# Kernel optimization log

Measured on AMD Instinct MI355X. Metric: run time of the kernel, lower is better.

The kernel has to match this reference:

```python
import jax, jax.numpy as jnp
import numpy as np

H = 64        # index_n_heads
D = 128       # index_head_dim
R = 64        # rope_head_dim
TOPK = 512    # index_topk
FP8_MAX = 448.0
EPS = 1e-6
THETA = 10000.0


def setup_inputs() -> dict:
    key = jax.random.key(0)
    ks = jax.random.split(key, 6)
    T, DM, QL = 1536, 7168, 1536
    return {
        "hidden_states": jax.random.normal(ks[0], (T, DM), jnp.float32),
        "q_lora": jax.random.normal(ks[1], (T, QL), jnp.float32),
        "wq_b": jax.random.normal(ks[2], (QL, H * D), jnp.float32) / np.sqrt(QL),
        "wk": jax.random.normal(ks[3], (DM, D), jnp.float32) / np.sqrt(DM),
        "k_norm_w": jnp.ones((D,), jnp.float32),
        "k_norm_b": jnp.zeros((D,), jnp.float32),
        "weights_proj_w": jax.random.normal(ks[4], (DM, H), jnp.float32) / np.sqrt(DM),
        "positions": jnp.arange(T, dtype=jnp.int32),
    }


def _rope_neox(x, pos):
    # x: [T, ..., R]; pos: [T]. NEOX-style (half-split) rotary on the rope slice.
    half = R // 2
    inv = 1.0 / (THETA ** (jnp.arange(half, dtype=jnp.float32) / half))
    ang = pos.astype(jnp.float32)[:, None] * inv  # [T, half]
    cos, sin = jnp.cos(ang), jnp.sin(ang)
    while cos.ndim < x.ndim:
        cos, sin = cos[:, None, :], sin[:, None, :]
    x1, x2 = x[..., :half], x[..., half:]
    return jnp.concatenate([x1 * cos - x2 * sin, x2 * cos + x1 * sin], axis=-1)


def _fp8_quant(x):
    # per-row (last-dim) e4m3 quantization: value -> fp8 payload + fp32 scale
    scale = jnp.maximum(jnp.max(jnp.abs(x), axis=-1, keepdims=True) / FP8_MAX, 1e-12)
    xq = (x / scale).astype(jnp.float8_e4m3fn).astype(jnp.float32)
    return xq, scale


def reference(hidden_states, q_lora, wq_b, wk, k_norm_w, k_norm_b, weights_proj_w, positions):
    T = hidden_states.shape[0]
    softmax_scale = D ** (-0.5)
    weights_scale = H ** (-0.5)

    # projections
    q = (q_lora @ wq_b).reshape(T, H, D)          # wq_b
    k = hidden_states @ wk                        # wk

    # k_norm (LayerNorm)
    mu = jnp.mean(k, axis=-1, keepdims=True)
    var = jnp.mean((k - mu) ** 2, axis=-1, keepdims=True)
    k = (k - mu) * jax.lax.rsqrt(var + EPS) * k_norm_w + k_norm_b

    # RoPE on the first rope_head_dim dims of q and k
    q = jnp.concatenate([_rope_neox(q[..., :R], positions), q[..., R:]], axis=-1)
    k = jnp.concatenate([_rope_neox(k[..., :R], positions), k[..., R:]], axis=-1)

    # fp8 quantization (per token-head for q, per token for k)
    q_fp8, q_scale = _fp8_quant(q)   # [T,H,D], [T,H,1]
    k_fp8, k_scale = _fp8_quant(k)   # [T,D],   [T,1]

    # head-gate weights: weights_proj(x) * q_scale * softmax_scale * weights_scale
    gate = hidden_states @ weights_proj_w                      # [T,H]
    w = gate[..., None] * q_scale * (softmax_scale * weights_scale)  # [T,H,1]

    # index score: I[t,s] = sum_h w[t,h] * relu(q[t,h] . k[s]) * k_scale[s]
    qk = jnp.einsum('thd,sd->ths', q_fp8, k_fp8)               # [T,H,S]
    score = jnp.einsum('th,ths->ts', w[..., 0], jax.nn.relu(qk))
    score = score * k_scale[:, 0][None, :]

    # causal (ragged prefill) mask + topk block selection
    causal = positions[:, None] >= positions[None, :]
    score = jnp.where(causal, score, -jnp.inf)
    vals, idx = jax.lax.top_k(score, TOPK)
    idx = jnp.where(jnp.isfinite(vals), idx, -1)
    return idx, vals
```

## Files before the change

kernel.cpp:

```cpp
#include <hip/hip_runtime.h>
#include <hip/hip_bf16.h>
#include <math.h>

#define T_SZ 1536
#define DM_SZ 7168
#define QL_SZ 1536
#define H_SZ 64
#define D_SZ 128
#define ND 8192
#define TOPK_SZ 512
#define N2 192
#define SPLITK2 16

typedef float f32x4 __attribute__((ext_vector_type(4)));
typedef short s16x8 __attribute__((ext_vector_type(8)));
typedef unsigned long long u64;

static __device__ __forceinline__ unsigned char f32_to_e4m3(float x){
  unsigned int b = __float_as_uint(x);
  unsigned int s = (b >> 24) & 0x80u;
  float a = fabsf(x);
  if (a < 0.015625f){
    int m = (int)rintf(a * 512.0f);
    if (m == 8) return (unsigned char)(s | 0x08u);
    return (unsigned char)(s | (unsigned)m);
  }
  int e;
  float mant = frexpf(a, &e);
  int E = e - 1;
  int m = (int)rintf(mant * 16.0f) - 8;
  if (m == 8){ E += 1; m = 0; }
  if (E > 8 || (E == 8 && m > 6)) return (unsigned char)(s | 0x7Eu);
  return (unsigned char)(s | ((unsigned)(E + 7) << 3) | (unsigned)m);
}

static __device__ __forceinline__ unsigned short bf16_rne(float x){
  unsigned int u = __float_as_uint(x);
  return (unsigned short)((u + 0x7FFFu + ((u >> 16) & 1u)) >> 16);
}

typedef __attribute__((address_space(1))) const void gas_void;
typedef __attribute__((address_space(3))) void las_void;
static __device__ __forceinline__ void stage16(const void* g, void* l){
  __builtin_amdgcn_global_load_lds((gas_void*)g, (las_void*)l, 16, 0, 0);
}

__global__ void rope_table_k(const int* __restrict__ pos, float* __restrict__ cs){
  int i = blockIdx.x * blockDim.x + threadIdx.x;
  if (i >= T_SZ * 32) return;
  int t = i >> 5, j = i & 31;
  float inv = 1.0f / powf(10000.0f, (float)j * (1.0f / 32.0f));
  float ang = (float)pos[t] * inv;
  cs[t * 64 + j]      = cosf(ang);
  cs[t * 64 + 32 + j] = sinf(ang);
}

__global__ __launch_bounds__(256) void conv_split_k(const float* __restrict__ A,
                                                    unsigned short* __restrict__ hi,
                                                    unsigned short* __restrict__ lo,
                                                    int n4){
  int i = blockIdx.x * 256 + threadIdx.x;
  if (i >= n4) return;
  float4 v = *(const float4*)&A[(size_t)i * 4];
  float f[4] = {v.x, v.y, v.z, v.w};
  unsigned short hb[4], lb[4];
#pragma unroll
  for (int j = 0; j < 4; ++j){
    hb[j] = bf16_rne(f[j]);
    float hf = __uint_as_float((unsigned int)hb[j] << 16);
    lb[j] = bf16_rne(f[j] - hf);
  }
  ushort4 h, l;
  h.x = hb[0]; h.y = hb[1]; h.z = hb[2]; h.w = hb[3];
  l.x = lb[0]; l.y = lb[1]; l.z = lb[2]; l.w = lb[3];
  *(ushort4*)&hi[(size_t)i * 4] = h;
  *(ushort4*)&lo[(size_t)i * 4] = l;
}

__global__ __launch_bounds__(256) void convB_k(const float* __restrict__ B,
                                               unsigned short* __restrict__ bhi,
                                               unsigned short* __restrict__ blo){
  __shared__ float ld[32][33];
  const int n0 = blockIdx.x * 32, k0 = blockIdx.y * 32;
  const int t = threadIdx.x;
  const int r = t >> 3, c4 = (t & 7) * 4;
  float4 v = *(const float4*)&B[(size_t)(k0 + r) * ND + n0 + c4];
  ld[r][c4 + 0] = v.x; ld[r][c4 + 1] = v.y; ld[r][c4 + 2] = v.z; ld[r][c4 + 3] = v.w;
  __syncthreads();
  unsigned short hb[4], lb[4];
#pragma unroll
  for (int j = 0; j < 4; ++j){
    float x = ld[c4 + j][r];
    hb[j] = bf16_rne(x);
    float hf = __uint_as_float((unsigned int)hb[j] << 16);
    lb[j] = bf16_rne(x - hf);
  }
  ushort4 h, l;
  h.x = hb[0]; h.y = hb[1]; h.z = hb[2]; h.w = hb[3];
  l.x = lb[0]; l.y = lb[1]; l.z = lb[2]; l.w = lb[3];
  *(ushort4*)&bhi[(size_t)(n0 + r) * QL_SZ + k0 + c4] = h;
  *(ushort4*)&blo[(size_t)(n0 + r) * QL_SZ + k0 + c4] = l;
}

__global__ __launch_bounds__(256) void conv_w2_k(const float* __restrict__ wk,
                                                 const float* __restrict__ wp,
                                                 unsigned short* __restrict__ bhi,
                                                 unsigned short* __restrict__ blo){
  __shared__ float ld[32][33];
  const int n0 = blockIdx.x * 32, k0 = blockIdx.y * 32;
  const int t = threadIdx.x;
  const int r = t >> 3, c4 = (t & 7) * 4;
  float4 v;
  if (n0 < 128) v = *(const float4*)&wk[(size_t)(k0 + r) * 128 + n0 + c4];
  else          v = *(const float4*)&wp[(size_t)(k0 + r) * 64 + (n0 - 128) + c4];
  ld[r][c4 + 0] = v.x; ld[r][c4 + 1] = v.y; ld[r][c4 + 2] = v.z; ld[r][c4 + 3] = v.w;
  __syncthreads();
  unsigned short hb[4], lb[4];
#pragma unroll
  for (int j = 0; j < 4; ++j){
    float x = ld[c4 + j][r];
    hb[j] = bf16_rne(x);
    float hf = __uint_as_float((unsigned int)hb[j] << 16);
    lb[j] = bf16_rne(x - hf);
  }
  ushort4 h, l;
  h.x = hb[0]; h.y = hb[1]; h.z = hb[2]; h.w = hb[3];
  l.x = lb[0]; l.y = lb[1]; l.z = lb[2]; l.w = lb[3];
  *(ushort4*)&bhi[(size_t)(n0 + r) * DM_SZ + k0 + c4] = h;
  *(ushort4*)&blo[(size_t)(n0 + r) * DM_SZ + k0 + c4] = l;
}

__global__ __launch_bounds__(256) void gemm1_mfma_k(const unsigned short* __restrict__ Ahi,
                                                    const unsigned short* __restrict__ Alo,
                                                    const unsigned short* __restrict__ Bhi,
                                                    const unsigned short* __restrict__ Blo,
                                                    float* __restrict__ C){
  __shared__ unsigned short As [128 * 64];
  __shared__ unsigned short Bs0[128 * 64];
  __shared__ unsigned short Bs1[128 * 64];
  const int bid = blockIdx.x;
  const int lid = (bid & 7) * 96 + (bid >> 3);
  const int mt = lid % 12, nt = lid / 12;
  const int m0 = mt * 128, n0 = nt * 128;
  const int tid = threadIdx.x;
  const int w = tid >> 6, l = tid & 63;
  const int wr = w >> 1, wc = w & 1;
  const int lr = l & 15, lg = l >> 4;

  const int srow = w * 32 + (l >> 3);
  const int ssl  = (l & 7) ^ ((l >> 3) & 7);
  const size_t gA = (size_t)(m0 + srow) * QL_SZ + ssl * 8;
  const size_t gB = (size_t)(n0 + srow) * QL_SZ + ssl * 8;
  const int lbase = w * 2048;

  f32x4 acc[4][4];
#pragma unroll
  for (int i = 0; i < 4; ++i)
#pragma unroll
    for (int j = 0; j < 4; ++j) acc[i][j] = (f32x4){0.f, 0.f, 0.f, 0.f};

  const int amrow = wr * 64 + lr;
  const int bnrow = wc * 64 + lr;

  for (int k0 = 0; k0 < QL_SZ; k0 += 64){
#pragma unroll
    for (int i = 0; i < 4; ++i){
      size_t go = (size_t)i * 8 * QL_SZ + k0;
      stage16(Ahi + gA + go, As  + lbase + i * 512);
      stage16(Bhi + gB + go, Bs0 + lbase + i * 512);
      stage16(Blo + gB + go, Bs1 + lbase + i * 512);
    }
    __syncthreads();
#pragma unroll
    for (int kk = 0; kk < 2; ++kk){
      s16x8 af[4], b0[4], b1[4];
#pragma unroll
      for (int f = 0; f < 4; ++f){
        int ma = amrow + f * 16;
        int nb = bnrow + f * 16;
        int sa = ((kk * 4 + lg) ^ (ma & 7)) * 16;
        int sb = ((kk * 4 + lg) ^ (nb & 7)) * 16;
        af[f] = *(const s16x8*)((const char*)As  + ma * 128 + sa);
        b0[f] = *(const s16x8*)((const char*)Bs0 + nb * 128 + sb);
        b1[f] = *(const s16x8*)((const char*)Bs1 + nb * 128 + sb);
      }
#pragma unroll
      for (int fi = 0; fi < 4; ++fi)
#pragma unroll
        for (int fj = 0; fj < 4; ++fj)
          acc[fi][fj] = __builtin_amdgcn_mfma_f32_16x16x32_bf16(af[fi], b0[fj], acc[fi][fj], 0, 0, 0);
#pragma unroll
      for (int fi = 0; fi < 4; ++fi)
#pragma unroll
        for (int fj = 0; fj < 4; ++fj)
          acc[fi][fj] = __builtin_amdgcn_mfma_f32_16x16x32_bf16(af[fi], b1[fj], acc[fi][fj], 0, 0, 0);
    }
    __syncthreads();
#pragma unroll
    for (int i = 0; i < 4; ++i)
      stage16(Alo + gA + (size_t)i * 8 * QL_SZ + k0, As + lbase + i * 512);
    __syncthreads();
#pragma unroll
    for (int kk = 0; kk < 2; ++kk){
      s16x8 af[4], b0[4];
#pragma unroll
      for (int f = 0; f < 4; ++f){
        int ma = amrow + f * 16;
        int nb = bnrow + f * 16;
        af[f] = *(const s16x8*)((const char*)As  + ma * 128 + (((kk * 4 + lg) ^ (ma & 7)) * 16));
        b0[f] = *(const s16x8*)((const char*)Bs0 + nb * 128 + (((kk * 4 + lg) ^ (nb & 7)) * 16));
      }
#pragma unroll
      for (int fi = 0; fi < 4; ++fi)
#pragma unroll
        for (int fj = 0; fj < 4; ++fj)
          acc[fi][fj] = __builtin_amdgcn_mfma_f32_16x16x32_bf16(af[fi], b0[fj], acc[fi][fj], 0, 0, 0);
    }
    __syncthreads();
  }

#pragma unroll
  for (int fi = 0; fi < 4; ++fi){
    const int row = m0 + wr * 64 + fi * 16 + lg * 4;
#pragma unroll
    for (int fj = 0; fj < 4; ++fj){
      float* cp = C + (size_t)row * ND + n0 + wc * 64 + fj * 16 + lr;
      f32x4 d = acc[fi][fj];
      cp[0]              = d.x;
      cp[(size_t)ND]     = d.y;
      cp[(size_t)2 * ND] = d.z;
      cp[(size_t)3 * ND] = d.w;
    }
  }
}

__global__ __launch_bounds__(128) void gemm2_mfma_k(const unsigned short* __restrict__ Ahi,
                                                    const unsigned short* __restrict__ Alo,
                                                    const unsigned short* __restrict__ Bhi,
                                                    const unsigned short* __restrict__ Blo,
                                                    float* __restrict__ part){
  __shared__ unsigned short As [128 * 64];
  __shared__ unsigned short Bs0[64 * 64];
  __shared__ unsigned short Bs1[64 * 64];
  const int bid = blockIdx.x;
  const int lid = (bid & 7) * 72 + (bid >> 3);
  const int s   = lid / 36;
  const int rem = lid % 36;
  const int mt = rem / 3, nt = rem % 3;
  const int m0 = mt * 128, n0 = nt * 64;
  const int kbeg = s * (DM_SZ / SPLITK2);
  const int tid = threadIdx.x;
  const int w = tid >> 6, l = tid & 63;
  const int lr = l & 15, lg = l >> 4;

  const int srow = tid >> 3;
  const int ssl  = (tid & 7) ^ (srow & 7);
  const size_t gA = (size_t)(m0 + srow) * DM_SZ + ssl * 8;
  const size_t gB = (size_t)(n0 + srow) * DM_SZ + ssl * 8;
  const int lbase = w * 512;

  f32x4 acc[4][4];
#pragma unroll
  for (int i = 0; i < 4; ++i)
#pragma unroll
    for (int j = 0; j < 4; ++j) acc[i][j] = (f32x4){0.f, 0.f, 0.f, 0.f};

  const int amrow = w * 64 + lr;
  const int bnrow = lr;

  for (int k0 = kbeg; k0 < kbeg + DM_SZ / SPLITK2; k0 += 64){
#pragma unroll
    for (int i = 0; i < 8; ++i)
      stage16(Ahi + gA + (size_t)i * 16 * DM_SZ + k0, As + lbase + i * 1024);
#pragma unroll
    for (int i = 0; i < 4; ++i){
      stage16(Bhi + gB + (size_t)i * 16 * DM_SZ + k0, Bs0 + lbase + i * 1024);
      stage16(Blo + gB + (size_t)i * 16 * DM_SZ + k0, Bs1 + lbase + i * 1024);
    }
    __syncthreads();
#pragma unroll
    for (int kk = 0; kk < 2; ++kk){
      s16x8 af[4], b0[4], b1[4];
#pragma unroll
      for (int f = 0; f < 4; ++f){
        int ma = amrow + f * 16;
        int nb = bnrow + f * 16;
        int sa = ((kk * 4 + lg) ^ (ma & 7)) * 16;
        int sb = ((kk * 4 + lg) ^ (nb & 7)) * 16;
        af[f] = *(const s16x8*)((const char*)As  + ma * 128 + sa);
        b0[f] = *(const s16x8*)((const char*)Bs0 + nb * 128 + sb);
        b1[f] = *(const s16x8*)((const char*)Bs1 + nb * 128 + sb);
      }
#pragma unroll
      for (int fi = 0; fi < 4; ++fi)
#pragma unroll
        for (int fj = 0; fj < 4; ++fj)
          acc[fi][fj] = __builtin_amdgcn_mfma_f32_16x16x32_bf16(af[fi], b0[fj], acc[fi][fj], 0, 0, 0);
#pragma unroll
      for (int fi = 0; fi < 4; ++fi)
#pragma unroll
        for (int fj = 0; fj < 4; ++fj)
          acc[fi][fj] = __builtin_amdgcn_mfma_f32_16x16x32_bf16(af[fi], b1[fj], acc[fi][fj], 0, 0, 0);
    }
    __syncthreads();
#pragma unroll
    for (int i = 0; i < 8; ++i)
      stage16(Alo + gA + (size_t)i * 16 * DM_SZ + k0, As + lbase + i * 1024);
    __syncthreads();
#pragma unroll
    for (int kk = 0; kk < 2; ++kk){
      s16x8 af[4], b0[4];
#pragma unroll
      for (int f = 0; f < 4; ++f){
        int ma = amrow + f * 16;
        int nb = bnrow + f * 16;
        af[f] = *(const s16x8*)((const char*)As  + ma * 128 + (((kk * 4 + lg) ^ (ma & 7)) * 16));
        b0[f] = *(const s16x8*)((const char*)Bs0 + nb * 128 + (((kk * 4 + lg) ^ (nb & 7)) * 16));
      }
#pragma unroll
      for (int fi = 0; fi < 4; ++fi)
#pragma unroll
        for (int fj = 0; fj < 4; ++fj)
          acc[fi][fj] = __builtin_amdgcn_mfma_f32_16x16x32_bf16(af[fi], b0[fj], acc[fi][fj], 0, 0, 0);
    }
    __syncthreads();
  }

  float* p = part + (size_t)(s * 36 + mt * 3 + nt) * (128 * 64);
#pragma unroll
  for (int fi = 0; fi < 4; ++fi){
    const int row = w * 64 + fi * 16 + lg * 4;
#pragma unroll
    for (int fj = 0; fj < 4; ++fj){
      float* cp = p + (size_t)row * 64 + fj * 16 + lr;
      f32x4 d = acc[fi][fj];
      cp[  0] = d.x;
      cp[ 64] = d.y;
      cp[128] = d.z;
      cp[192] = d.w;
    }
  }
}

__global__ void gemm2_reduce2_k(const float* __restrict__ part,
                                float* __restrict__ kraw, float* __restrict__ gate){
  int e = blockIdx.x * 256 + threadIdx.x;
  if (e >= T_SZ * N2) return;
  int r = e / N2, c = e % N2;
  int mt = r >> 7, rl = r & 127;
  int nt = c >> 6, cl = c & 63;
  const float* pp = part + (size_t)(mt * 3 + nt) * (128 * 64) + rl * 64 + cl;
  float sum = 0.0f;
#pragma unroll
  for (int s = 0; s < SPLITK2; ++s) sum += pp[(size_t)s * 36 * 128 * 64];
  if (c < 128) kraw[r * 128 + c] = sum;
  else         gate[r * 64 + (c - 128)] = sum;
}

__global__ __launch_bounds__(256) void gemm1_k(const float* __restrict__ A,
                                               const float* __restrict__ B,
                                               float* __restrict__ C){
  __shared__ float As[8][132];
  __shared__ float Bs[8][132];
  const int tid = threadIdx.x;
  const int bm = blockIdx.y * 128, bn = blockIdx.x * 128;
  const int ty = tid >> 4, tx = tid & 15;
  const int arow = tid >> 1, ak = (tid & 1) * 4;
  const int brow = tid >> 5, bcol = (tid & 31) * 4;
  float acc[8][8];
#pragma unroll
  for (int i = 0; i < 8; i++)
#pragma unroll
    for (int j = 0; j < 8; j++) acc[i][j] = 0.0f;

  for (int k0 = 0; k0 < QL_SZ; k0 += 8){
    float4 av = *(const float4*)&A[(size_t)(bm + arow) * QL_SZ + k0 + ak];
    float4 bv = *(const float4*)&B[(size_t)(k0 + brow) * ND + bn + bcol];
    As[ak + 0][arow] = av.x; As[ak + 1][arow] = av.y;
    As[ak + 2][arow] = av.z; As[ak + 3][arow] = av.w;
    *(float4*)&Bs[brow][bcol] = bv;
    __syncthreads();
#pragma unroll
    for (int kk = 0; kk < 8; ++kk){
      float a[8], b[8];
      *(float4*)&a[0] = *(const float4*)&As[kk][ty * 8];
      *(float4*)&a[4] = *(const float4*)&As[kk][ty * 8 + 4];
      *(float4*)&b[0] = *(const float4*)&Bs[kk][tx * 8];
      *(float4*)&b[4] = *(const float4*)&Bs[kk][tx * 8 + 4];
#pragma unroll
      for (int i = 0; i < 8; i++)
#pragma unroll
        for (int j = 0; j < 8; j++) acc[i][j] += a[i] * b[j];
    }
    __syncthreads();
  }
#pragma unroll
  for (int i = 0; i < 8; i++)
#pragma unroll
    for (int j = 0; j < 8; j += 4){
      float4 o; o.x = acc[i][j]; o.y = acc[i][j+1]; o.z = acc[i][j+2]; o.w = acc[i][j+3];
      *(float4*)&C[(size_t)(bm + ty * 8 + i) * ND + bn + tx * 8 + j] = o;
    }
}

__global__ __launch_bounds__(256) void gemm2_partial_k(const float* __restrict__ hs,
                                                       const float* __restrict__ wk,
                                                       const float* __restrict__ wp,
                                                       float* __restrict__ part){
  __shared__ float As[32][33];
  __shared__ float Bs[32][196];
  const int tid = threadIdx.x;
  const int m0 = blockIdx.x * 32;
  const int ks = blockIdx.y;
  const int kbeg = ks * (DM_SZ / 8), kend = kbeg + DM_SZ / 8;
  const int arow = tid >> 3, ak4 = (tid & 7) * 4;
  const int r2 = (tid >> 4) * 2, cg = (tid & 15) * 12;
  float acc[2][12];
#pragma unroll
  for (int i = 0; i < 2; i++)
#pragma unroll
    for (int j = 0; j < 12; j++) acc[i][j] = 0.0f;

  for (int k0 = kbeg; k0 < kend; k0 += 32){
    float4 av = *(const float4*)&hs[(size_t)(m0 + arow) * DM_SZ + k0 + ak4];
    As[ak4 + 0][arow] = av.x; As[ak4 + 1][arow] = av.y;
    As[ak4 + 2][arow] = av.z; As[ak4 + 3][arow] = av.w;
#pragma unroll
    for (int i = 0; i < 6; ++i){
      int fi = tid + i * 256;
      int row = fi / 48, c4 = fi % 48;
      float4 bv;
      if (c4 < 32) bv = *(const float4*)&wk[(size_t)(k0 + row) * 128 + c4 * 4];
      else         bv = *(const float4*)&wp[(size_t)(k0 + row) * 64 + (c4 - 32) * 4];
      *(float4*)&Bs[row][c4 * 4] = bv;
    }
    __syncthreads();
#pragma unroll
    for (int kk = 0; kk < 32; ++kk){
      float a0 = As[kk][r2], a1 = As[kk][r2 + 1];
      float b[12];
      *(float4*)&b[0] = *(const float4*)&Bs[kk][cg];
      *(float4*)&b[4] = *(const float4*)&Bs[kk][cg + 4];
      *(float4*)&b[8] = *(const float4*)&Bs[kk][cg + 8];
#pragma unroll
      for (int j = 0; j < 12; j++){ acc[0][j] += a0 * b[j]; acc[1][j] += a1 * b[j]; }
    }
    __syncthreads();
  }
  float* p = part + (size_t)(ks * 48 + blockIdx.x) * 32 * 192;
#pragma unroll
  for (int i = 0; i < 2; i++)
#pragma unroll
    for (int j = 0; j < 12; j += 4){
      float4 o; o.x = acc[i][j]; o.y = acc[i][j+1]; o.z = acc[i][j+2]; o.w = acc[i][j+3];
      *(float4*)&p[(r2 + i) * 192 + cg + j] = o;
    }
}

__global__ void gemm2_reduce_k(const float* __restrict__ part,
                               float* __restrict__ kraw, float* __restrict__ gate){
  int e = blockIdx.x * 256 + threadIdx.x;
  if (e >= T_SZ * 192) return;
  int r = e / 192, c = e % 192;
  int mt = r >> 5, rl = r & 31;
  float s = 0.0f;
  for (int ks = 0; ks < 8; ++ks)
    s += part[((size_t)(ks * 48 + mt) * 32 + rl) * 192 + c];
  if (c < 128) kraw[r * 128 + c] = s;
  else         gate[r * 64 + (c - 128)] = s;
}

__global__ __launch_bounds__(128) void k_post_k(const float* __restrict__ kraw,
                                                const float* __restrict__ knw,
                                                const float* __restrict__ knb,
                                                const float* __restrict__ cs,
                                                unsigned char* __restrict__ kf8,
                                                float* __restrict__ kscale){
  const int t = blockIdx.x, d = threadIdx.x;
  __shared__ float sh[128];
  __shared__ float red[2];
  float x = kraw[t * 128 + d];
  float v = x;
#pragma unroll
  for (int o = 32; o > 0; o >>= 1) v += __shfl_xor(v, o, 64);
  if ((d & 63) == 0) red[d >> 6] = v;
  __syncthreads();
  float mu = (red[0] + red[1]) / 128.0f;
  float dx = x - mu;
  v = dx * dx;
  __syncthreads();
#pragma unroll
  for (int o = 32; o > 0; o >>= 1) v += __shfl_xor(v, o, 64);
  if ((d & 63) == 0) red[d >> 6] = v;
  __syncthreads();
  float var = (red[0] + red[1]) / 128.0f;
  float nv = dx * (1.0f / sqrtf(var + 1e-6f)) * knw[d] + knb[d];
  sh[d] = nv;
  __syncthreads();
  float outv;
  const float* ct = cs + t * 64;
  if (d < 32)        outv = nv * ct[d] - sh[d + 32] * ct[32 + d];
  else if (d < 64){ int j = d - 32; outv = nv * ct[j] + sh[j] * ct[32 + j]; }
  else               outv = nv;
  v = fabsf(outv);
  __syncthreads();
#pragma unroll
  for (int o = 32; o > 0; o >>= 1) v = fmaxf(v, __shfl_xor(v, o, 64));
  if ((d & 63) == 0) red[d >> 6] = v;
  __syncthreads();
  float amax = fmaxf(red[0], red[1]);
  float scale = fmaxf(amax / 448.0f, 1e-12f);
  kf8[t * 128 + d] = f32_to_e4m3(outv / scale);
  if (d == 0) kscale[t] = scale;
}

__global__ __launch_bounds__(128) void q_post_k(const float* __restrict__ q,
                                                const float* __restrict__ gate,
                                                const float* __restrict__ cs,
                                                unsigned char* __restrict__ qf8,
                                                float* __restrict__ wbuf){
  const int row = blockIdx.x;
  const int d = threadIdx.x;
  const int t = row >> 6;
  __shared__ float sh[128];
  __shared__ float red[2];
  float x = q[(size_t)row * 128 + d];
  sh[d] = x;
  __syncthreads();
  float outv;
  const float* ct = cs + t * 64;
  if (d < 32)        outv = x * ct[d] - sh[d + 32] * ct[32 + d];
  else if (d < 64){ int j = d - 32; outv = x * ct[j] + sh[j] * ct[32 + j]; }
  else               outv = x;
  float v = fabsf(outv);
#pragma unroll
  for (int o = 32; o > 0; o >>= 1) v = fmaxf(v, __shfl_xor(v, o, 64));
  if ((d & 63) == 0) red[d >> 6] = v;
  __syncthreads();
  float amax = fmaxf(red[0], red[1]);
  float scale = fmaxf(amax / 448.0f, 1e-12f);
  qf8[(size_t)row * 128 + d] = f32_to_e4m3(outv / scale);
  if (d == 0) wbuf[row] = gate[row] * scale * 0.011048543456039806f;
}

__global__ __launch_bounds__(256) void score_mfma_k(const unsigned char* __restrict__ qf8,
                                                    const unsigned char* __restrict__ kf8,
                                                    const float* __restrict__ wbuf,
                                                    const float* __restrict__ kscale,
                                                    float* __restrict__ score){
  const int bt = blockIdx.y, bs = blockIdx.x;
  if (bs > bt) return;
  const int t0 = bt * 64, s0 = bs * 64;
  const int tid = threadIdx.x;
  const int w  = tid >> 6;
  const int l  = tid & 63;
  const int lr = l & 15;
  const int lg = l >> 4;

  __shared__ float wl[64][68];
#pragma unroll
  for (int i = 0; i < 4; i++){
    int fi = tid + i * 256;
    int row = fi >> 4, c4 = (fi & 15) * 4;
    *(float4*)&wl[row][c4] = *(const float4*)&wbuf[(t0 + row) * 64 + c4];
  }

  u64 b00,b01,b02,b03, b10,b11,b12,b13, b20,b21,b22,b23, b30,b31,b32,b33;
  {
    const unsigned char* kb = kf8 + (size_t)s0 * 128 + 8 * lg;
    const unsigned char* k0r = kb + (size_t)(lr     ) * 128;
    const unsigned char* k1r = kb + (size_t)(lr + 16) * 128;
    const unsigned char* k2r = kb + (size_t)(lr + 32) * 128;
    const unsigned char* k3r = kb + (size_t)(lr + 48) * 128;
    b00=*(const u64*)(k0r+0);  b01=*(const u64*)(k0r+32); b02=*(const u64*)(k0r+64); b03=*(const u64*)(k0r+96);
    b10=*(const u64*)(k1r+0);  b11=*(const u64*)(k1r+32); b12=*(const u64*)(k1r+64); b13=*(const u64*)(k1r+96);
    b20=*(const u64*)(k2r+0);  b21=*(const u64*)(k2r+32); b22=*(const u64*)(k2r+64); b23=*(const u64*)(k2r+96);
    b30=*(const u64*)(k3r+0);  b31=*(const u64*)(k3r+32); b32=*(const u64*)(k3r+64); b33=*(const u64*)(k3r+96);
  }
  __syncthreads();

  const unsigned char* qp = qf8 + (size_t)(t0 + 16 * w + lr) * 8192 + 8 * lg;
  u64 a0 = *(const u64*)(qp +  0), a1 = *(const u64*)(qp + 32),
      a2 = *(const u64*)(qp + 64), a3 = *(const u64*)(qp + 96);

  f32x4 acc0 = {0,0,0,0}, acc1 = {0,0,0,0}, acc2 = {0,0,0,0}, acc3 = {0,0,0,0};
  const int wrow = 16 * w + 4 * lg;

  for (int h = 0; h < 64; ++h){
    const unsigned char* qn = qp + ((h + 1) & 63) * 128;
    u64 p0 = *(const u64*)(qn +  0), p1 = *(const u64*)(qn + 32),
        p2 = *(const u64*)(qn + 64), p3 = *(const u64*)(qn + 96);

    f32x4 c0 = {0,0,0,0}, c1 = {0,0,0,0}, c2 = {0,0,0,0}, c3 = {0,0,0,0};
    c0 = __builtin_amdgcn_mfma_f32_16x16x32_fp8_fp8((long)a0, (long)b00, c0, 0, 0, 0);
    c1 = __builtin_amdgcn_mfma_f32_16x16x32_fp8_fp8((long)a0, (long)b10, c1, 0, 0, 0);
    c2 = __builtin_amdgcn_mfma_f32_16x16x32_fp8_fp8((long)a0, (long)b20, c2, 0, 0, 0);
    c3 = __builtin_amdgcn_mfma_f32_16x16x32_fp8_fp8((long)a0, (long)b30, c3, 0, 0, 0);
    c0 = __builtin_amdgcn_mfma_f32_16x16x32_fp8_fp8((long)a1, (long)b01, c0, 0, 0, 0);
    c1 = __builtin_amdgcn_mfma_f32_16x16x32_fp8_fp8((long)a1, (long)b11, c1, 0, 0, 0);
    c2 = __builtin_amdgcn_mfma_f32_16x16x32_fp8_fp8((long)a1, (long)b21, c2, 0, 0, 0);
    c3 = __builtin_amdgcn_mfma_f32_16x16x32_fp8_fp8((long)a1, (long)b31, c3, 0, 0, 0);
    c0 = __builtin_amdgcn_mfma_f32_16x16x32_fp8_fp8((long)a2, (long)b02, c0, 0, 0, 0);
    c1 = __builtin_amdgcn_mfma_f32_16x16x32_fp8_fp8((long)a2, (long)b12, c1, 0, 0, 0);
    c2 = __builtin_amdgcn_mfma_f32_16x16x32_fp8_fp8((long)a2, (long)b22, c2, 0, 0, 0);
    c3 = __builtin_amdgcn_mfma_f32_16x16x32_fp8_fp8((long)a2, (long)b32, c3, 0, 0, 0);
    c0 = __builtin_amdgcn_mfma_f32_16x16x32_fp8_fp8((long)a3, (long)b03, c0, 0, 0, 0);
    c1 = __builtin_amdgcn_mfma_f32_16x16x32_fp8_fp8((long)a3, (long)b13, c1, 0, 0, 0);
    c2 = __builtin_amdgcn_mfma_f32_16x16x32_fp8_fp8((long)a3, (long)b23, c2, 0, 0, 0);
    c3 = __builtin_amdgcn_mfma_f32_16x16x32_fp8_fp8((long)a3, (long)b33, c3, 0, 0, 0);

    float w0 = wl[wrow + 0][h], w1 = wl[wrow + 1][h],
          w2 = wl[wrow + 2][h], w3 = wl[wrow + 3][h];
    acc0.x += w0 * fmaxf(c0.x, 0.0f); acc0.y += w1 * fmaxf(c0.y, 0.0f);
    acc0.z += w2 * fmaxf(c0.z, 0.0f); acc0.w += w3 * fmaxf(c0.w, 0.0f);
    acc1.x += w0 * fmaxf(c1.x, 0.0f); acc1.y += w1 * fmaxf(c1.y, 0.0f);
    acc1.z += w2 * fmaxf(c1.z, 0.0f); acc1.w += w3 * fmaxf(c1.w, 0.0f);
    acc2.x += w0 * fmaxf(c2.x, 0.0f); acc2.y += w1 * fmaxf(c2.y, 0.0f);
    acc2.z += w2 * fmaxf(c2.z, 0.0f); acc2.w += w3 * fmaxf(c2.w, 0.0f);
    acc3.x += w0 * fmaxf(c3.x, 0.0f); acc3.y += w1 * fmaxf(c3.y, 0.0f);
    acc3.z += w2 * fmaxf(c3.z, 0.0f); acc3.w += w3 * fmaxf(c3.w, 0.0f);

    a0 = p0; a1 = p1; a2 = p2; a3 = p3;
  }

  const int trow = t0 + 16 * w + 4 * lg;
  float ks0 = kscale[s0 + lr], ks1 = kscale[s0 + 16 + lr],
        ks2 = kscale[s0 + 32 + lr], ks3 = kscale[s0 + 48 + lr];
  float* sp0 = score + (size_t)(trow + 0) * T_SZ + s0 + lr;
  float* sp1 = score + (size_t)(trow + 1) * T_SZ + s0 + lr;
  float* sp2 = score + (size_t)(trow + 2) * T_SZ + s0 + lr;
  float* sp3 = score + (size_t)(trow + 3) * T_SZ + s0 + lr;
  sp0[ 0] = acc0.x * ks0; sp1[ 0] = acc0.y * ks0; sp2[ 0] = acc0.z * ks0; sp3[ 0] = acc0.w * ks0;
  sp0[16] = acc1.x * ks1; sp1[16] = acc1.y * ks1; sp2[16] = acc1.z * ks1; sp3[16] = acc1.w * ks1;
  sp0[32] = acc2.x * ks2; sp1[32] = acc2.y * ks2; sp2[32] = acc2.z * ks2; sp3[32] = acc2.w * ks2;
  sp0[48] = acc3.x * ks3; sp1[48] = acc3.y * ks3; sp2[48] = acc3.z * ks3; sp3[48] = acc3.w * ks3;
}

__global__ __launch_bounds__(256) void topk_sel_k(const float* __restrict__ score,
                                                  float* __restrict__ out){
  const int t = blockIdx.x, tid = threadIdx.x;
  const int n = t + 1;
  __shared__ unsigned int U[2048];
  __shared__ unsigned long long cand[512];
  __shared__ unsigned int hist[256];
  __shared__ unsigned int tix[1536];
  __shared__ unsigned int cnts[2];
  __shared__ unsigned int sel[2];

  const float* srow = score + (size_t)t * T_SZ;
#pragma unroll
  for (int m = 0; m < 8; ++m){
    int j = tid + m * 256;
    unsigned int u = 0u;
    if (j < n){
      unsigned int b = __float_as_uint(srow[j]);
      u = (b & 0x80000000u) ? ~b : (b | 0x80000000u);
    }
    U[j] = u;
  }
  if (tid < 2) cnts[tid] = 0u;
  __syncthreads();

  if (n > 512){
    unsigned int prefix = 0u, rem = 512u;
#pragma unroll
    for (int level = 0; level < 4; ++level){
      const int shift = 24 - 8 * level;
      hist[tid] = 0u;
      __syncthreads();
#pragma unroll
      for (int m = 0; m < 8; ++m){
        unsigned int u = U[tid + m * 256];
        bool match = (u != 0u) && (level == 0 || (u >> (shift + 8)) == prefix);
        if (match) atomicAdd(&hist[(u >> shift) & 255u], 1u);
      }
      __syncthreads();
      if (tid < 64){
        unsigned int c0 = hist[tid*4], c1 = hist[tid*4+1], c2 = hist[tid*4+2], c3 = hist[tid*4+3];
        unsigned int loc = c0 + c1 + c2 + c3;
        unsigned int acc = loc;
        for (int off = 1; off < 64; off <<= 1){
          unsigned int v = __shfl_down(acc, off, 64);
          if (tid + off < 64) acc += v;
        }
        unsigned int S3 = acc - loc;
        unsigned int S2 = S3 + c3;
        unsigned int S1 = S2 + c2;
        unsigned int S0 = S1 + c1;
        if (S0 < rem && rem <= S0 + c0){ sel[0] = tid*4 + 0; sel[1] = S0; }
        if (S1 < rem && rem <= S1 + c1){ sel[0] = tid*4 + 1; sel[1] = S1; }
        if (S2 < rem && rem <= S2 + c2){ sel[0] = tid*4 + 2; sel[1] = S2; }
        if (S3 < rem && rem <= S3 + c3){ sel[0] = tid*4 + 3; sel[1] = S3; }
      }
      __syncthreads();
      prefix = (prefix << 8) | sel[0];
      rem -= sel[1];
    }
    const unsigned int u_thr = prefix;

#pragma unroll
    for (int m = 0; m < 8; ++m){
      int j = tid + m * 256;
      unsigned int u = U[j];
      if (u > u_thr){
        unsigned int p = atomicAdd(&cnts[0], 1u);
        cand[p] = ((unsigned long long)u << 32) | (unsigned int)(~(unsigned int)j);
      } else if (u == u_thr){
        unsigned int q = atomicAdd(&cnts[1], 1u);
        tix[q] = (unsigned int)j;
      }
    }
    __syncthreads();
    const unsigned int G = cnts[0], Tt = cnts[1];
    if (Tt == rem){
      for (unsigned int q = tid; q < Tt; q += 256)
        cand[G + q] = ((unsigned long long)u_thr << 32) | (unsigned int)(~tix[q]);
      __syncthreads();
    } else {
      if (tid < 64) hist[tid] = 0u;
      __syncthreads();
      for (unsigned int q = tid; q < Tt; q += 256) atomicAdd(&hist[tix[q] >> 5], 1u);
      __syncthreads();
      if (tid == 0){
        unsigned int cum = 0; unsigned int d = 0;
        for (; d < 64; ++d){ unsigned int c = hist[d]; if (cum + c >= rem) break; cum += c; }
        sel[0] = d; sel[1] = rem - cum;
      }
      __syncthreads();
      const unsigned int dA = sel[0], remA = sel[1];
      if (tid < 32) hist[64 + tid] = 0u;
      __syncthreads();
      for (unsigned int q = tid; q < Tt; q += 256){
        unsigned int j = tix[q];
        if ((j >> 5) == dA) atomicAdd(&hist[64 + (j & 31u)], 1u);
      }
      __syncthreads();
      if (tid == 0){
        unsigned int cum = 0; unsigned int e = 0;
        for (; e < 32; ++e){ unsigned int c = hist[64 + e]; if (cum + c >= remA) break; cum += c; }
        sel[0] = dA * 32 + e;
        cnts[1] = 0u;
      }
      __syncthreads();
      const unsigned int jthr = sel[0];
      for (unsigned int q = tid; q < Tt; q += 256){
        unsigned int j = tix[q];
        if (j <= jthr){
          unsigned int p = atomicAdd(&cnts[1], 1u);
          cand[G + p] = ((unsigned long long)u_thr << 32) | (unsigned int)(~j);
        }
      }
      __syncthreads();
    }
  } else {
    for (int i = tid; i < 512; i += 256){
      unsigned int u = (i < n) ? U[i] : 0u;
      cand[i] = u ? (((unsigned long long)u << 32) | (unsigned int)(~(unsigned int)i)) : 0ull;
    }
    __syncthreads();
  }

  for (int k = 2; k <= 512; k <<= 1){
    for (int j = k >> 1; j > 0; j >>= 1){
#pragma unroll
      for (int m = 0; m < 2; ++m){
        int i = tid + m * 256;
        int ixj = i ^ j;
        if (ixj > i){
          unsigned long long A = cand[i], B = cand[ixj];
          bool up = (i & k) == 0;
          if (up ? (A < B) : (A > B)){ cand[i] = B; cand[ixj] = A; }
        }
      }
      __syncthreads();
    }
  }

  for (int i = tid; i < TOPK_SZ; i += 256){
    unsigned long long kk = cand[i];
    unsigned int u = (unsigned int)(kk >> 32);
    unsigned int b = (u & 0x80000000u) ? (u & 0x7fffffffu) : ~u;
    float val = __uint_as_float(b);
    int idx = (int)(~(unsigned int)(kk & 0xffffffffu));
    bool fin = (u != 0u) && (val > -__builtin_huge_valf());
    out[(size_t)t * TOPK_SZ + i] = fin ? (float)idx : -1.0f;
    out[(size_t)T_SZ * TOPK_SZ + (size_t)t * TOPK_SZ + i] = fin ? val : -3.0e38f;
  }
}

extern "C" void kernel_launch(void* const* d_in, const int* in_sizes, int n_in,
                              void* d_out, int out_size, void* d_ws, size_t ws_size,
                              hipStream_t stream){
  const float* hs  = (const float*)d_in[0];
  const float* ql  = (const float*)d_in[1];
  const float* wqb = (const float*)d_in[2];
  const float* wk  = (const float*)d_in[3];
  const float* knw = (const float*)d_in[4];
  const float* knb = (const float*)d_in[5];
  const float* wpj = (const float*)d_in[6];
  const int*   pos = (const int*)d_in[7];
  char* ws = (char*)d_ws;
  size_t off = 0;
  auto alloc = [&](size_t b){ size_t o = off; off += (b + 255) & ~(size_t)255; return o; };
  float* cs     = (float*)(ws + alloc((size_t)T_SZ * 64 * 4));
  float* qbuf   = (float*)(ws + alloc((size_t)T_SZ * ND * 4));
  float* kraw   = (float*)(ws + alloc((size_t)T_SZ * 128 * 4));
  float* gate   = (float*)(ws + alloc((size_t)T_SZ * 64 * 4));
  unsigned char* kf8 = (unsigned char*)(ws + alloc((size_t)T_SZ * 128));
  float* kscale = (float*)(ws + alloc((size_t)T_SZ * 4));
  float* wbuf   = (float*)(ws + alloc((size_t)T_SZ * 64 * 4));
  const size_t base2 = off;

  size_t oA = base2;
  auto allocA = [&](size_t b){ size_t o = oA; oA += (b + 255) & ~(size_t)255; return o; };
  unsigned short* hshi = (unsigned short*)(ws + allocA((size_t)T_SZ * DM_SZ * 2));
  unsigned short* hslo = (unsigned short*)(ws + allocA((size_t)T_SZ * DM_SZ * 2));
  unsigned short* w2hi = (unsigned short*)(ws + allocA((size_t)N2 * DM_SZ * 2));
  unsigned short* w2lo = (unsigned short*)(ws + allocA((size_t)N2 * DM_SZ * 2));
  float* part2 = (float*)(ws + allocA((size_t)SPLITK2 * 36 * 128 * 64 * 4));
  const bool fitA = (oA <= ws_size);

  size_t oB = base2;
  auto allocB = [&](size_t b){ size_t o = oB; oB += (b + 255) & ~(size_t)255; return o; };
  unsigned short* Ahi = (unsigned short*)(ws + allocB((size_t)T_SZ * QL_SZ * 2));
  unsigned short* Alo = (unsigned short*)(ws + allocB((size_t)T_SZ * QL_SZ * 2));
  unsigned short* Bth = (unsigned short*)(ws + allocB((size_t)ND * QL_SZ * 2));
  unsigned short* Btl = (unsigned short*)(ws + allocB((size_t)ND * QL_SZ * 2));
  const bool fitB = (oB <= ws_size);

  unsigned char* qf8 = (unsigned char*)(ws + base2);
  float* part_old    = (float*)(ws + base2);
  float* score = qbuf;
  float* out = (float*)d_out;

  rope_table_k<<<dim3((T_SZ * 32 + 255) / 256), dim3(256), 0, stream>>>(pos, cs);

  if (fitA){
    conv_split_k<<<dim3(T_SZ * DM_SZ / 4 / 256), dim3(256), 0, stream>>>(hs, hshi, hslo, T_SZ * DM_SZ / 4);
    conv_w2_k<<<dim3(N2 / 32, DM_SZ / 32), dim3(256), 0, stream>>>(wk, wpj, w2hi, w2lo);
    gemm2_mfma_k<<<dim3(12 * 3 * SPLITK2), dim3(128), 0, stream>>>(hshi, hslo, w2hi, w2lo, part2);
    gemm2_reduce2_k<<<dim3((T_SZ * N2 + 255) / 256), dim3(256), 0, stream>>>(part2, kraw, gate);
  } else {
    gemm2_partial_k<<<dim3(48, 8), dim3(256), 0, stream>>>(hs, wk, wpj, part_old);
    gemm2_reduce_k<<<dim3((T_SZ * 192) / 256), dim3(256), 0, stream>>>(part_old, kraw, gate);
  }
  k_post_k<<<dim3(T_SZ), dim3(128), 0, stream>>>(kraw, knw, knb, cs, kf8, kscale);

  if (fitB){
    conv_split_k<<<dim3(T_SZ * QL_SZ / 4 / 256), dim3(256), 0, stream>>>(ql, Ahi, Alo, T_SZ * QL_SZ / 4);
    convB_k<<<dim3(ND / 32, QL_SZ / 32), dim3(256), 0, stream>>>(wqb, Bth, Btl);
    gemm1_mfma_k<<<dim3(768), dim3(256), 0, stream>>>(Ahi, Alo, Bth, Btl, qbuf);
  } else {
    gemm1_k<<<dim3(ND / 128, T_SZ / 128), dim3(256), 0, stream>>>(ql, wqb, qbuf);
  }
  q_post_k<<<dim3(T_SZ * H_SZ), dim3(128), 0, stream>>>(qbuf, gate, cs, qf8, wbuf);

  score_mfma_k<<<dim3(24, 24), dim3(256), 0, stream>>>(qf8, kf8, wbuf, kscale, score);
  topk_sel_k<<<dim3(T_SZ), dim3(256), 0, stream>>>(score, out);
}
```

Measured before the change: 313.1 us.

## Split score kernel over head halves with triangular block indexing

The score kernel now launches only the 300 lower-triangular tile pairs, using a linear index mapped to (bt,bs), instead of a 24x24 grid where half the blocks exit immediately. Each tile pair is further split into two blocks that each handle 32 heads, which doubles parallelism. Each half writes its partial score to a separate buffer, and the top-k kernel sums the two partials when it loads a row. This adds a second T×T score buffer and doubles score write and read traffic. The score buffer must be large enough to hold both halves, which is not visible here.

Measured after the change: 302.7 us. 3.3% less time.

```diff
diff --git a/kernel.cpp b/kernel.cpp
--- a/kernel.cpp
+++ b/kernel.cpp
@@ -548,8 +548,13 @@
                                                     const float* __restrict__ wbuf,
                                                     const float* __restrict__ kscale,
                                                     float* __restrict__ score){
-  const int bt = blockIdx.y, bs = blockIdx.x;
-  if (bs > bt) return;
+  const int bid = blockIdx.x;
+  const int p = bid >> 1;
+  const int h0 = (bid & 1) * 32;
+  int bt = (int)((sqrtf(8.0f * (float)p + 1.0f) - 1.0f) * 0.5f);
+  while ((bt + 1) * (bt + 2) / 2 <= p) ++bt;
+  while (bt * (bt + 1) / 2 > p) --bt;
+  const int bs = p - bt * (bt + 1) / 2;
   const int t0 = bt * 64, s0 = bs * 64;
   const int tid = threadIdx.x;
   const int w  = tid >> 6;
@@ -579,15 +584,15 @@
   }
   __syncthreads();
 
-  const unsigned char* qp = qf8 + (size_t)(t0 + 16 * w + lr) * 8192 + 8 * lg;
+  const unsigned char* qp = qf8 + (size_t)(t0 + 16 * w + lr) * 8192 + h0 * 128 + 8 * lg;
   u64 a0 = *(const u64*)(qp +  0), a1 = *(const u64*)(qp + 32),
       a2 = *(const u64*)(qp + 64), a3 = *(const u64*)(qp + 96);
 
   f32x4 acc0 = {0,0,0,0}, acc1 = {0,0,0,0}, acc2 = {0,0,0,0}, acc3 = {0,0,0,0};
   const int wrow = 16 * w + 4 * lg;
 
-  for (int h = 0; h < 64; ++h){
-    const unsigned char* qn = qp + ((h + 1) & 63) * 128;
+  for (int h = 0; h < 32; ++h){
+    const unsigned char* qn = qp + ((h + 1) & 31) * 128;
     u64 p0 = *(const u64*)(qn +  0), p1 = *(const u64*)(qn + 32),
         p2 = *(const u64*)(qn + 64), p3 = *(const u64*)(qn + 96);
 
@@ -609,8 +614,8 @@
     c2 = __builtin_amdgcn_mfma_f32_16x16x32_fp8_fp8((long)a3, (long)b23, c2, 0, 0, 0);
     c3 = __builtin_amdgcn_mfma_f32_16x16x32_fp8_fp8((long)a3, (long)b33, c3, 0, 0, 0);
 
-    float w0 = wl[wrow + 0][h], w1 = wl[wrow + 1][h],
-          w2 = wl[wrow + 2][h], w3 = wl[wrow + 3][h];
+    float w0 = wl[wrow + 0][h0 + h], w1 = wl[wrow + 1][h0 + h],
+          w2 = wl[wrow + 2][h0 + h], w3 = wl[wrow + 3][h0 + h];
     acc0.x += w0 * fmaxf(c0.x, 0.0f); acc0.y += w1 * fmaxf(c0.y, 0.0f);
     acc0.z += w2 * fmaxf(c0.z, 0.0f); acc0.w += w3 * fmaxf(c0.w, 0.0f);
     acc1.x += w0 * fmaxf(c1.x, 0.0f); acc1.y += w1 * fmaxf(c1.y, 0.0f);
@@ -626,10 +631,11 @@
   const int trow = t0 + 16 * w + 4 * lg;
   float ks0 = kscale[s0 + lr], ks1 = kscale[s0 + 16 + lr],
         ks2 = kscale[s0 + 32 + lr], ks3 = kscale[s0 + 48 + lr];
-  float* sp0 = score + (size_t)(trow + 0) * T_SZ + s0 + lr;
-  float* sp1 = score + (size_t)(trow + 1) * T_SZ + s0 + lr;
-  float* sp2 = score + (size_t)(trow + 2) * T_SZ + s0 + lr;
-  float* sp3 = score + (size_t)(trow + 3) * T_SZ + s0 + lr;
+  float* sbase = score + (size_t)(bid & 1) * T_SZ * T_SZ;
+  float* sp0 = sbase + (size_t)(trow + 0) * T_SZ + s0 + lr;
+  float* sp1 = sbase + (size_t)(trow + 1) * T_SZ + s0 + lr;
+  float* sp2 = sbase + (size_t)(trow + 2) * T_SZ + s0 + lr;
+  float* sp3 = sbase + (size_t)(trow + 3) * T_SZ + s0 + lr;
   sp0[ 0] = acc0.x * ks0; sp1[ 0] = acc0.y * ks0; sp2[ 0] = acc0.z * ks0; sp3[ 0] = acc0.w * ks0;
   sp0[16] = acc1.x * ks1; sp1[16] = acc1.y * ks1; sp2[16] = acc1.z * ks1; sp3[16] = acc1.w * ks1;
   sp0[32] = acc2.x * ks2; sp1[32] = acc2.y * ks2; sp2[32] = acc2.z * ks2; sp3[32] = acc2.w * ks2;
@@ -647,13 +653,15 @@
   __shared__ unsigned int cnts[2];
   __shared__ unsigned int sel[2];
 
-  const float* srow = score + (size_t)t * T_SZ;
+  const float* s0row = score + (size_t)t * T_SZ;
+  const float* s1row = score + (size_t)T_SZ * T_SZ + (size_t)t * T_SZ;
 #pragma unroll
   for (int m = 0; m < 8; ++m){
     int j = tid + m * 256;
     unsigned int u = 0u;
     if (j < n){
-      unsigned int b = __float_as_uint(srow[j]);
+      float val = s0row[j] + s1row[j];
+      unsigned int b = __float_as_uint(val);
       u = (b & 0x80000000u) ? ~b : (b | 0x80000000u);
     }
     U[j] = u;
@@ -855,6 +863,6 @@
   }
   q_post_k<<<dim3(T_SZ * H_SZ), dim3(128), 0, stream>>>(qbuf, gate, cs, qf8, wbuf);
 
-  score_mfma_k<<<dim3(24, 24), dim3(256), 0, stream>>>(qf8, kf8, wbuf, kscale, score);
+  score_mfma_k<<<dim3(600), dim3(256), 0, stream>>>(qf8, kf8, wbuf, kscale, score);
   topk_sel_k<<<dim3(T_SZ), dim3(256), 0, stream>>>(score, out);
 }
```
